# Performance work log

Measured on AMD Instinct MI355X. Metric: run time of the kernel, lower is better.

The kernel has to match this reference:

```python
import jax, jax.numpy as jnp
import numpy as np

B, A, C = 1, 196416, 90
H = W = 1024
SCORE_THRESHOLD = 0.05
MAX_DETECTIONS = 100
# RetinaNet-style BBoxTransform normalization (mean=0, std=[0.1,0.1,0.2,0.2])
STD = (0.1, 0.1, 0.2, 0.2)


def setup_inputs() -> dict:
    key = jax.random.key(0)
    k1, k2, k3, k4, k5, k6, k7 = jax.random.split(key, 7)
    x = jax.random.normal(k1, (B, 3, H, W), dtype=jnp.float32)
    regression = jax.random.normal(k2, (B, A, 4), dtype=jnp.float32) * 0.1
    classification = jax.random.normal(k3, (B, A, C), dtype=jnp.float32)
    # valid anchor boxes (x1, y1, x2, y2)
    cx = jax.random.uniform(k4, (B, A), minval=0.0, maxval=float(W))
    cy = jax.random.uniform(k5, (B, A), minval=0.0, maxval=float(H))
    aw = jax.random.uniform(k6, (B, A), minval=16.0, maxval=256.0)
    ah = jax.random.uniform(k7, (B, A), minval=16.0, maxval=256.0)
    anchors = jnp.stack([cx - 0.5 * aw, cy - 0.5 * ah, cx + 0.5 * aw, cy + 0.5 * ah], axis=2).astype(jnp.float32)
    return {"x": x, "regression": regression, "classification": classification, "anchors": anchors}


def _decode_clip(anchors, regression, img_h, img_w):
    # BBoxTransform: deltas (dx, dy, dw, dh) scaled by std, applied to anchor center/size
    wa = anchors[..., 2] - anchors[..., 0]
    ha = anchors[..., 3] - anchors[..., 1]
    cxa = anchors[..., 0] + 0.5 * wa
    cya = anchors[..., 1] + 0.5 * ha
    dx = regression[..., 0] * STD[0]
    dy = regression[..., 1] * STD[1]
    dw = regression[..., 2] * STD[2]
    dh = regression[..., 3] * STD[3]
    cx = cxa + dx * wa
    cy = cya + dy * ha
    w = jnp.exp(dw) * wa
    h = jnp.exp(dh) * ha
    # ClipBoxes: x1,y1 clamped at 0; x2,y2 clamped at image width/height
    x1 = jnp.maximum(cx - 0.5 * w, 0.0)
    y1 = jnp.maximum(cy - 0.5 * h, 0.0)
    x2 = jnp.minimum(cx + 0.5 * w, float(img_w))
    y2 = jnp.minimum(cy + 0.5 * h, float(img_h))
    return jnp.stack([x1, y1, x2, y2], axis=2)  # [B, A, 4]


def reference(x, regression, classification, anchors):
    img_h, img_w = x.shape[2], x.shape[3]
    boxes = _decode_clip(anchors, regression, img_h, img_w)  # [1, A, 4]
    probs = jax.nn.sigmoid(classification)                    # [1, A, C]
    scores = jnp.max(probs, axis=2)                           # [1, A]
    classes = jnp.argmax(probs, axis=2)                       # [1, A]
    valid_scores = jnp.where(scores > SCORE_THRESHOLD, scores, 0.0)
    vb = boxes[0]            # [A, 4]
    vc = classes[0]          # [A]
    vs = valid_scores[0]     # [A]
    k = min(MAX_DETECTIONS, vs.shape[0])
    _, top_idx = jax.lax.top_k(vs, k)
    final_boxes = vb[top_idx]
    final_scores = vs[top_idx]
    final_classes = vc[top_idx]
    return (final_boxes, final_scores, final_classes)
```

## Files before the change

### kernel.cpp

```cpp
#include <hip/hip_runtime.h>
#include <cmath>

#define A_CNT 196416
#define C_CNT 90
#define TOT_ELEMS (A_CNT * C_CNT)
#define TOPK 100u
#define AB 128
#define NB_REDUCE ((A_CNT + AB - 1) / AB)

#define OFF_HIST1 785664u
#define OFF_HIST2 789760u
#define OFF_CTRL  1051904u
#define OFF_CAND  1051968u
#define OFF_EQ    1052480u
#define WS_END    1056576u

__global__ __launch_bounds__(256) void k_reduce(const float* __restrict__ cls,
                                                unsigned* __restrict__ keys,
                                                unsigned* __restrict__ hist1) {
    __shared__ alignas(16) float smem[AB * C_CNT];
    __shared__ unsigned lhist[1024];
    const int t = threadIdx.x;
    for (int j = t; j < 1024; j += 256) lhist[j] = 0u;

    const int base = blockIdx.x * (AB * C_CNT);
    const int nvc = min(AB * C_CNT, TOT_ELEMS - base) >> 2;
    const float4* __restrict__ g4 = (const float4*)(cls + base);
    float4* __restrict__ s4 = (float4*)smem;
    for (int c = t; c < nvc; c += 256) s4[c] = g4[c];
    __syncthreads();

    const int r = t >> 1;
    const int h = t & 1;
    const int a = blockIdx.x * AB + r;
    float m = -INFINITY;
    if (a < A_CNT) {
        const float2* q = (const float2*)(smem + r * C_CNT + (h ? 48 : 0));
        const int n2 = h ? 21 : 24;
        for (int i = 0; i < n2; ++i) {
            float2 p = q[i];
            m = fmaxf(m, fmaxf(p.x, p.y));
        }
    }
    float om = __shfl_xor(m, 1);
    m = fmaxf(m, om);
    if (h == 0 && a < A_CNT) {
        float prob = 1.0f / (1.0f + expf(-m));
        unsigned key = (prob > 0.05f) ? __float_as_uint(prob) : 0u;
        keys[a] = key;
        unsigned hidx = key ? (min(key >> 16, 0x3F80u) - 0x3D4Bu) : 0u;
        atomicAdd(&lhist[hidx], 1u);
    }
    __syncthreads();
    for (int j = t; j < 1024; j += 256) {
        unsigned c = lhist[j];
        if (c) atomicAdd(&hist1[j], c);
    }
}

template <int CHUNK>
__global__ __launch_bounds__(256) void k_scan(const unsigned* __restrict__ hist,
                                              unsigned* __restrict__ ctrl, int mode) {
    __shared__ unsigned sdata[256];
    __shared__ unsigned sbin[2];
    const int t = threadIdx.x;
    const unsigned target = TOPK;
    const unsigned above0 = (mode == 0) ? 0u : ctrl[1];

    unsigned s = 0;
    const uint4* p = (const uint4*)(hist + t * CHUNK);
#pragma unroll 8
    for (int j = 0; j < CHUNK / 4; ++j) { uint4 u = p[j]; s += u.x + u.y + u.z + u.w; }
    sdata[t] = s;
    for (int d = 1; d < 256; d <<= 1) {
        __syncthreads();
        unsigned add = (t + d < 256) ? sdata[t + d] : 0u;
        __syncthreads();
        sdata[t] += add;
    }
    __syncthreads();
    {
        unsigned mysuf  = sdata[t] + above0;
        unsigned nxtsuf = ((t < 255) ? sdata[t + 1] : 0u) + above0;
        if (nxtsuf < target && mysuf >= target) { sbin[0] = (unsigned)t; sbin[1] = nxtsuf - above0; }
    }
    __syncthreads();
    const unsigned chunkB = sbin[0];
    const unsigned gAbove = sbin[1] + above0;

    unsigned v = (t < CHUNK) ? hist[chunkB * CHUNK + t] : 0u;
    sdata[t] = v;
    for (int d = 1; d < 256; d <<= 1) {
        __syncthreads();
        unsigned add = (t + d < 256) ? sdata[t + d] : 0u;
        __syncthreads();
        sdata[t] += add;
    }
    __syncthreads();
    {
        unsigned mysuf  = sdata[t] + gAbove;
        unsigned nxtsuf = ((t < 255) ? sdata[t + 1] : 0u) + gAbove;
        if (nxtsuf < target && mysuf >= target) {
            unsigned bin = chunkB * CHUNK + (unsigned)t;
            if (mode == 0) {
                ctrl[0] = bin ? (bin + 0x3D4Bu) : 0u;
                ctrl[1] = nxtsuf;
            } else {
                ctrl[2] = (ctrl[0] << 16) | bin;
                ctrl[3] = nxtsuf;
                ctrl[4] = target - nxtsuf;
            }
        }
    }
}

__global__ __launch_bounds__(256) void k_hist2(const unsigned* __restrict__ keys,
                                               const unsigned* __restrict__ ctrl,
                                               unsigned* __restrict__ hist2) {
    const unsigned binB = ctrl[0];
    int i = blockIdx.x * 256 + threadIdx.x;
    const int n = gridDim.x * 256;
    for (; i < A_CNT; i += n) {
        unsigned k = keys[i];
        if ((k >> 16) == binB) atomicAdd(&hist2[k & 0xFFFFu], 1u);
    }
}

__global__ __launch_bounds__(256) void k_gather(const unsigned* __restrict__ keys,
                                                unsigned* __restrict__ ctrl,
                                                unsigned* __restrict__ cand,
                                                unsigned* __restrict__ eqi) {
    const unsigned T = ctrl[2];
    int i = blockIdx.x * 256 + threadIdx.x;
    const int n = gridDim.x * 256;
    for (; i < A_CNT; i += n) {
        unsigned k = keys[i];
        if (k > T) {
            unsigned p = atomicAdd(&ctrl[5], 1u);
            if (p < 128u) cand[p] = (unsigned)i;
        } else if (k == T) {
            unsigned p = atomicAdd(&ctrl[6], 1u);
            if (p < 1024u) eqi[p] = (unsigned)i;
        }
    }
}

__global__ __launch_bounds__(128) void k_final(const float* __restrict__ cls,
                                               const float* __restrict__ reg,
                                               const float* __restrict__ anc,
                                               const unsigned* __restrict__ ctrl,
                                               const unsigned* __restrict__ cand,
                                               const unsigned* __restrict__ eqi,
                                               const unsigned* __restrict__ keys,
                                               float* __restrict__ out) {
    __shared__ unsigned sel[TOPK];
    const int t = threadIdx.x;
    const unsigned n_gt = ctrl[3];
    const unsigned need_eq = ctrl[4];
    unsigned eq_cnt = ctrl[6];
    if (eq_cnt > 1024u) eq_cnt = 1024u;

    if (t < (int)n_gt) {
        unsigned mi = cand[t], mk = keys[mi], r = 0;
        for (unsigned j = 0; j < n_gt; ++j) {
            unsigned oj = cand[j], ok = keys[oj];
            if (ok > mk || (ok == mk && oj < mi)) r++;
        }
        sel[r] = mi;
    }
    for (unsigned e = (unsigned)t; e < eq_cnt; e += 128u) {
        unsigned mi = eqi[e], r = 0;
        for (unsigned j = 0; j < eq_cnt; ++j)
            if (eqi[j] < mi) r++;
        if (r < need_eq) sel[n_gt + r] = mi;
    }
    __syncthreads();

    if (t < (int)TOPK) {
        const unsigned a = sel[t];
        const float* row = cls + (size_t)a * C_CNT;
        float bv = -INFINITY; int bi = 0;
        for (int c = 0; c < C_CNT; ++c) {
            float v = row[c];
            if (v > bv) { bv = v; bi = c; }
        }
        float score = __uint_as_float(keys[a]);
        float x1a = anc[a * 4 + 0], y1a = anc[a * 4 + 1];
        float x2a = anc[a * 4 + 2], y2a = anc[a * 4 + 3];
        float wa = x2a - x1a, ha = y2a - y1a;
        float cxa = x1a + 0.5f * wa, cya = y1a + 0.5f * ha;
        float dx = reg[a * 4 + 0] * 0.1f, dy = reg[a * 4 + 1] * 0.1f;
        float dw = reg[a * 4 + 2] * 0.2f, dh = reg[a * 4 + 3] * 0.2f;
        float cx = cxa + dx * wa, cy = cya + dy * ha;
        float w = expf(dw) * wa, h = expf(dh) * ha;
        out[t * 4 + 0] = fmaxf(cx - 0.5f * w, 0.0f);
        out[t * 4 + 1] = fmaxf(cy - 0.5f * h, 0.0f);
        out[t * 4 + 2] = fminf(cx + 0.5f * w, 1024.0f);
        out[t * 4 + 3] = fminf(cy + 0.5f * h, 1024.0f);
        out[400 + t] = score;
        out[500 + t] = (float)bi;
    }
}

extern "C" void kernel_launch(void* const* d_in, const int* in_sizes, int n_in,
                              void* d_out, int out_size, void* d_ws, size_t ws_size,
                              hipStream_t stream) {
    const float* reg = (const float*)d_in[1];
    const float* cls = (const float*)d_in[2];
    const float* anc = (const float*)d_in[3];
    float* out = (float*)d_out;
    char* ws = (char*)d_ws;
    unsigned* keys  = (unsigned*)ws;
    unsigned* hist1 = (unsigned*)(ws + OFF_HIST1);
    unsigned* hist2 = (unsigned*)(ws + OFF_HIST2);
    unsigned* ctrl  = (unsigned*)(ws + OFF_CTRL);
    unsigned* cand  = (unsigned*)(ws + OFF_CAND);
    unsigned* eqi   = (unsigned*)(ws + OFF_EQ);

    hipMemsetAsync(ws + OFF_HIST1, 0, WS_END - OFF_HIST1, stream);
    k_reduce<<<NB_REDUCE, 256, 0, stream>>>(cls, keys, hist1);
    k_scan<4><<<1, 256, 0, stream>>>(hist1, ctrl, 0);
    k_hist2<<<256, 256, 0, stream>>>(keys, ctrl, hist2);
    k_scan<256><<<1, 256, 0, stream>>>(hist2, ctrl, 1);
    k_gather<<<256, 256, 0, stream>>>(keys, ctrl, cand, eqi);
    k_final<<<1, 128, 0, stream>>>(cls, reg, anc, ctrl, cand, eqi, keys, out);
}
```

Baseline: 165.1 us.

## Read class rows directly per anchor pair, fold hist2 zeroing into reduce

The reduce kernel drops its shared-memory staging. Each thread now reads two anchor rows (180 floats, 45 float4) straight from global memory and computes both maxima, shrinking LDS use and the local histogram to 576 bins. Clearing hist2 moves into the reduce kernel, so the large memset becomes two small ones. The hist2 and gather kernels read keys as uint4 with one pass per thread, and the final argmax reads float2. Per-thread strided float4 loads are less coalesced than the earlier cooperative copy, which risks lower effective memory bandwidth.

```diff
diff --git a/kernel.cpp b/kernel.cpp
--- a/kernel.cpp
+++ b/kernel.cpp
@@ -3,56 +3,58 @@
 
 #define A_CNT 196416
 #define C_CNT 90
-#define TOT_ELEMS (A_CNT * C_CNT)
+#define PAIRS (A_CNT / 2)
 #define TOPK 100u
-#define AB 128
-#define NB_REDUCE ((A_CNT + AB - 1) / AB)
+#define RB 128
+#define NB_REDUCE ((PAIRS + RB - 1) / RB)
 
 #define OFF_HIST1 785664u
 #define OFF_HIST2 789760u
 #define OFF_CTRL  1051904u
 #define OFF_CAND  1051968u
 #define OFF_EQ    1052480u
-#define WS_END    1056576u
-
-__global__ __launch_bounds__(256) void k_reduce(const float* __restrict__ cls,
-                                                unsigned* __restrict__ keys,
-                                                unsigned* __restrict__ hist1) {
-    __shared__ alignas(16) float smem[AB * C_CNT];
-    __shared__ unsigned lhist[1024];
+
+__global__ __launch_bounds__(RB) void k_reduce(const float* __restrict__ cls,
+                                               unsigned* __restrict__ keys,
+                                               unsigned* __restrict__ hist1,
+                                               unsigned* __restrict__ hist2) {
+    __shared__ unsigned lhist[576];
     const int t = threadIdx.x;
-    for (int j = t; j < 1024; j += 256) lhist[j] = 0u;
-
-    const int base = blockIdx.x * (AB * C_CNT);
-    const int nvc = min(AB * C_CNT, TOT_ELEMS - base) >> 2;
-    const float4* __restrict__ g4 = (const float4*)(cls + base);
-    float4* __restrict__ s4 = (float4*)smem;
-    for (int c = t; c < nvc; c += 256) s4[c] = g4[c];
-    __syncthreads();
-
-    const int r = t >> 1;
-    const int h = t & 1;
-    const int a = blockIdx.x * AB + r;
-    float m = -INFINITY;
-    if (a < A_CNT) {
-        const float2* q = (const float2*)(smem + r * C_CNT + (h ? 48 : 0));
-        const int n2 = h ? 21 : 24;
-        for (int i = 0; i < n2; ++i) {
-            float2 p = q[i];
-            m = fmaxf(m, fmaxf(p.x, p.y));
-        }
-    }
-    float om = __shfl_xor(m, 1);
-    m = fmaxf(m, om);
-    if (h == 0 && a < A_CNT) {
-        float prob = 1.0f / (1.0f + expf(-m));
-        unsigned key = (prob > 0.05f) ? __float_as_uint(prob) : 0u;
-        keys[a] = key;
-        unsigned hidx = key ? (min(key >> 16, 0x3F80u) - 0x3D4Bu) : 0u;
-        atomicAdd(&lhist[hidx], 1u);
-    }
-    __syncthreads();
-    for (int j = t; j < 1024; j += 256) {
+    for (int j = t; j < 576; j += RB) lhist[j] = 0u;
+    __syncthreads();
+
+    const int p = blockIdx.x * RB + t;
+    if (p < PAIRS) {
+        const float4* __restrict__ r4 = (const float4*)cls + (size_t)p * 45;
+        float m0 = -INFINITY, m1;
+#pragma unroll
+        for (int i = 0; i < 22; ++i) {
+            float4 v = r4[i];
+            m0 = fmaxf(m0, fmaxf(fmaxf(v.x, v.y), fmaxf(v.z, v.w)));
+        }
+        {
+            float4 v = r4[22];
+            m0 = fmaxf(m0, fmaxf(v.x, v.y));
+            m1 = fmaxf(v.z, v.w);
+        }
+#pragma unroll
+        for (int i = 23; i < 45; ++i) {
+            float4 v = r4[i];
+            m1 = fmaxf(m1, fmaxf(fmaxf(v.x, v.y), fmaxf(v.z, v.w)));
+        }
+        float p0 = 1.0f / (1.0f + expf(-m0));
+        float p1 = 1.0f / (1.0f + expf(-m1));
+        unsigned k0 = (p0 > 0.05f) ? __float_as_uint(p0) : 0u;
+        unsigned k1 = (p1 > 0.05f) ? __float_as_uint(p1) : 0u;
+        *(uint2*)(keys + 2 * p) = make_uint2(k0, k1);
+        unsigned h0 = k0 ? (min(k0 >> 16, 0x3F80u) - 0x3D4Bu) : 0u;
+        unsigned h1 = k1 ? (min(k1 >> 16, 0x3F80u) - 0x3D4Bu) : 0u;
+        atomicAdd(&lhist[h0], 1u);
+        atomicAdd(&lhist[h1], 1u);
+        if (p < 65536) hist2[p] = 0u;
+    }
+    __syncthreads();
+    for (int j = t; j < 576; j += RB) {
         unsigned c = lhist[j];
         if (c) atomicAdd(&hist1[j], c);
     }
@@ -118,12 +120,13 @@
                                                const unsigned* __restrict__ ctrl,
                                                unsigned* __restrict__ hist2) {
     const unsigned binB = ctrl[0];
-    int i = blockIdx.x * 256 + threadIdx.x;
-    const int n = gridDim.x * 256;
-    for (; i < A_CNT; i += n) {
-        unsigned k = keys[i];
-        if ((k >> 16) == binB) atomicAdd(&hist2[k & 0xFFFFu], 1u);
-    }
+    const int i4 = blockIdx.x * 256 + threadIdx.x;
+    if (i4 >= A_CNT / 4) return;
+    uint4 k = ((const uint4*)keys)[i4];
+    if ((k.x >> 16) == binB) atomicAdd(&hist2[k.x & 0xFFFFu], 1u);
+    if ((k.y >> 16) == binB) atomicAdd(&hist2[k.y & 0xFFFFu], 1u);
+    if ((k.z >> 16) == binB) atomicAdd(&hist2[k.z & 0xFFFFu], 1u);
+    if ((k.w >> 16) == binB) atomicAdd(&hist2[k.w & 0xFFFFu], 1u);
 }
 
 __global__ __launch_bounds__(256) void k_gather(const unsigned* __restrict__ keys,
@@ -131,16 +134,19 @@
                                                 unsigned* __restrict__ cand,
                                                 unsigned* __restrict__ eqi) {
     const unsigned T = ctrl[2];
-    int i = blockIdx.x * 256 + threadIdx.x;
-    const int n = gridDim.x * 256;
-    for (; i < A_CNT; i += n) {
-        unsigned k = keys[i];
-        if (k > T) {
-            unsigned p = atomicAdd(&ctrl[5], 1u);
-            if (p < 128u) cand[p] = (unsigned)i;
-        } else if (k == T) {
-            unsigned p = atomicAdd(&ctrl[6], 1u);
-            if (p < 1024u) eqi[p] = (unsigned)i;
+    const int i4 = blockIdx.x * 256 + threadIdx.x;
+    if (i4 >= A_CNT / 4) return;
+    uint4 k = ((const uint4*)keys)[i4];
+    const unsigned base = (unsigned)(4 * i4);
+#pragma unroll
+    for (int j = 0; j < 4; ++j) {
+        unsigned kk = (j == 0) ? k.x : (j == 1) ? k.y : (j == 2) ? k.z : k.w;
+        if (kk > T) {
+            unsigned q = atomicAdd(&ctrl[5], 1u);
+            if (q < 128u) cand[q] = base + j;
+        } else if (kk == T) {
+            unsigned q = atomicAdd(&ctrl[6], 1u);
+            if (q < 1024u) eqi[q] = base + j;
         }
     }
 }
@@ -178,11 +184,13 @@
 
     if (t < (int)TOPK) {
         const unsigned a = sel[t];
-        const float* row = cls + (size_t)a * C_CNT;
+        const float2* row = (const float2*)(cls + (size_t)a * C_CNT);
         float bv = -INFINITY; int bi = 0;
-        for (int c = 0; c < C_CNT; ++c) {
-            float v = row[c];
-            if (v > bv) { bv = v; bi = c; }
+#pragma unroll 5
+        for (int c = 0; c < 45; ++c) {
+            float2 v = row[c];
+            if (v.x > bv) { bv = v.x; bi = 2 * c; }
+            if (v.y > bv) { bv = v.y; bi = 2 * c + 1; }
         }
         float score = __uint_as_float(keys[a]);
         float x1a = anc[a * 4 + 0], y1a = anc[a * 4 + 1];
@@ -217,11 +225,12 @@
     unsigned* cand  = (unsigned*)(ws + OFF_CAND);
     unsigned* eqi   = (unsigned*)(ws + OFF_EQ);
 
-    hipMemsetAsync(ws + OFF_HIST1, 0, WS_END - OFF_HIST1, stream);
-    k_reduce<<<NB_REDUCE, 256, 0, stream>>>(cls, keys, hist1);
+    hipMemsetAsync(hist1, 0, 1024 * 4, stream);
+    hipMemsetAsync(ctrl, 0, 64, stream);
+    k_reduce<<<NB_REDUCE, RB, 0, stream>>>(cls, keys, hist1, hist2);
     k_scan<4><<<1, 256, 0, stream>>>(hist1, ctrl, 0);
-    k_hist2<<<256, 256, 0, stream>>>(keys, ctrl, hist2);
+    k_hist2<<<192, 256, 0, stream>>>(keys, ctrl, hist2);
     k_scan<256><<<1, 256, 0, stream>>>(hist2, ctrl, 1);
-    k_gather<<<256, 256, 0, stream>>>(keys, ctrl, cand, eqi);
+    k_gather<<<192, 256, 0, stream>>>(keys, ctrl, cand, eqi);
     k_final<<<1, 128, 0, stream>>>(cls, reg, anc, ctrl, cand, eqi, keys, out);
 }
```

Result: no change. 165.8 us (+0.4%).
